# Kernel optimization log

Measured on AMD Instinct MI355X. Metric: run time of the kernel, lower is better.

The kernel has to match this reference:

```python
import jax, jax.numpy as jnp
import numpy as np

B, C, N, H, S = 2048, 64, 64, 8, 4
D = C // H          # head dim 8
CS = C // S         # per-scale channels 16
CP = C // 4         # pattern memory dim 16


def _conv1d(x, w, b):
    # x: [B, Cin, N], w: [Cout, Cin, 3], 'same' padding
    y = jax.lax.conv_general_dilated(x, w, (1,), ((1, 1),),
                                     dimension_numbers=('NCH', 'OIH', 'NCH'))
    return y + b[None, :, None]


def setup_inputs() -> dict:
    key = jax.random.key(0)
    ks = jax.random.split(key, 20)
    s = 0.05
    f32 = jnp.float32
    return {
        'x': jax.random.normal(ks[0], (B, C, N), f32),
        'points': jax.random.normal(ks[1], (N, 3), f32),
        'conv1_w': jax.random.normal(ks[2], (S, CS, C, 3), f32) * s,
        'conv1_b': jnp.zeros((S, CS), f32),
        'conv2_w': jax.random.normal(ks[3], (S, CS, CS, 3), f32) * s,
        'conv2_b': jnp.zeros((S, CS), f32),
        'pattern_memory': jax.random.normal(ks[4], (64, CP), f32),
        'pm1_w': jax.random.normal(ks[5], (C, C + CP), f32) * s,
        'pm1_b': jnp.zeros((C,), f32),
        'pm2_w': jax.random.normal(ks[6], (C, C), f32) * s,
        'pm2_b': jnp.zeros((C,), f32),
        'q_w': jax.random.normal(ks[7], (C, C), f32) * s,
        'q_b': jnp.zeros((C,), f32),
        'k_w': jax.random.normal(ks[8], (C, C), f32) * s,
        'k_b': jnp.zeros((C,), f32),
        'v_w': jax.random.normal(ks[9], (C, C), f32) * s,
        'v_b': jnp.zeros((C,), f32),
        'in_w': jax.random.normal(ks[10], (3 * C, C), f32) * s,
        'in_b': jnp.zeros((3 * C,), f32),
        'mo_w': jax.random.normal(ks[11], (C, C), f32) * s,
        'mo_b': jnp.zeros((C,), f32),
        'out_w': jax.random.normal(ks[12], (C, C), f32) * s,
        'out_b': jnp.zeros((C,), f32),
        'ln_g': jnp.ones((C,), f32),
        'ln_beta': jnp.zeros((C,), f32),
        'adjacency': jax.random.randint(ks[13], (64, 64), 0, 2, jnp.int32),
    }


def _forward(x, points, conv1_w, conv1_b, conv2_w, conv2_b, pattern_memory,
             pm1_w, pm1_b, pm2_w, pm2_b, q_w, q_b, k_w, k_b, v_w, v_b,
             in_w, in_b, mo_w, mo_b, out_w, out_b, ln_g, ln_beta, adjacency):
    b, c, n = x.shape
    # multi-scale conv stacks (fixed small loop over scales)
    feats = []
    for i in range(S):
        y = jax.nn.relu(_conv1d(x, conv1_w[i], conv1_b[i]))
        y = jax.nn.relu(_conv1d(y, conv2_w[i], conv2_b[i]))
        feats.append(jnp.transpose(y, (0, 2, 1)))  # [B, N, CS]
    combined = jnp.concatenate(feats, axis=-1)     # [B, N, C]
    # pattern memory broadcast per point (N == 64)
    pat = jnp.broadcast_to(pattern_memory[None], (b, n, CP))
    pi = jnp.concatenate([combined, pat], axis=-1)  # [B, N, C+CP]
    pf = jax.nn.relu(pi @ pm1_w.T + pm1_b) @ pm2_w.T + pm2_b  # [B, N, C]
    q = pf @ q_w.T + q_b
    k = pf @ k_w.T + k_b
    v = pf @ v_w.T + v_b
    # nn.MultiheadAttention: internal in_proj + out_proj
    wq, wk, wv = in_w[:C], in_w[C:2 * C], in_w[2 * C:]
    bq, bk, bv = in_b[:C], in_b[C:2 * C], in_b[2 * C:]
    q2 = (q @ wq.T + bq).reshape(b, n, H, D)
    k2 = (k @ wk.T + bk).reshape(b, n, H, D)
    v2 = (v @ wv.T + bv).reshape(b, n, H, D)
    scale = 1.0 / np.sqrt(D).astype(np.float32)
    scores = jnp.einsum('bnhd,bmhd->bhnm', q2, k2) * scale
    attn = jax.nn.softmax(scores, axis=-1)
    ctx = jnp.einsum('bhnm,bmhd->bnhd', attn, v2).reshape(b, n, C)
    attended = ctx @ mo_w.T + mo_b
    # vectorized geometric bias (replaces the 64x64 python loop)
    diff = points[:, None, :] - points[None, :, :]
    dist = jnp.sqrt(jnp.sum(diff * diff, axis=-1) + 1e-12)
    geo = jnp.where(adjacency > 0, jnp.float32(0.5), -0.1 / (1.0 + dist))
    attended = attended + geo[None]
    # layer norm over channels, then output projection
    h = attended + pf
    mu = jnp.mean(h, axis=-1, keepdims=True)
    var = jnp.mean((h - mu) ** 2, axis=-1, keepdims=True)
    hn = (h - mu) * jax.lax.rsqrt(var + 1e-5) * ln_g + ln_beta
    out = hn @ out_w.T + out_b
    return jnp.transpose(out, (0, 2, 1))  # [B, C, N]


def reference(x, points, conv1_w, conv1_b, conv2_w, conv2_b, pattern_memory,
              pm1_w, pm1_b, pm2_w, pm2_b, q_w, q_b, k_w, k_b, v_w, v_b,
              in_w, in_b, mo_w, mo_b, out_w, out_b, ln_g, ln_beta, adjacency):
    return _forward(x, points, conv1_w, conv1_b, conv2_w, conv2_b,
                    pattern_memory, pm1_w, pm1_b, pm2_w, pm2_b, q_w, q_b,
                    k_w, k_b, v_w, v_b, in_w, in_b, mo_w, mo_b, out_w, out_b,
                    ln_g, ln_beta, adjacency)
```

## Files before the change

kernel.cpp:

```cpp
#include <hip/hip_runtime.h>
#include <math.h>

using bf16x8 = __attribute__((ext_vector_type(8))) __bf16;
using f32x4  = __attribute__((ext_vector_type(4))) float;

#if __has_builtin(__builtin_amdgcn_exp2f)
#define EXP2F(x) __builtin_amdgcn_exp2f(x)
#else
#define EXP2F(x) exp2f(x)
#endif

__device__ __forceinline__ unsigned short f2bf(float f) {
  unsigned u = __float_as_uint(f);
  unsigned r = u + 0x7fffu + ((u >> 16) & 1u);
  return (unsigned short)(r >> 16);
}

__device__ __forceinline__ unsigned cvt_pk_bf16(float a, float b) {
  unsigned r;
  asm("v_cvt_pk_bf16_f32 %0, %1, %2" : "=v"(r) : "v"(a), "v"(b));
  return r;
}
__device__ __forceinline__ uint2 pk4(float a, float b, float c, float d) {
  uint2 r; r.x = cvt_pk_bf16(a, b); r.y = cvt_pk_bf16(c, d); return r;
}

__device__ __forceinline__ f32x4 mfma16(uint4 a, uint4 b, f32x4 c) {
  return __builtin_amdgcn_mfma_f32_16x16x32_bf16(
      __builtin_bit_cast(bf16x8, a), __builtin_bit_cast(bf16x8, b), c, 0, 0, 0);
}
__device__ __forceinline__ float swz_xor16(float v) {
  return __int_as_float(__builtin_amdgcn_ds_swizzle(__float_as_int(v), 0x401F));
}

#define FRAG_OFF(k, n) (((((n) >> 4) * 2 + ((k) >> 5)) * 64 + (((k) >> 3) & 3) * 16 + ((n) & 15)) * 8 + ((k) & 7))

#define ATT_C 0.51006997f

__global__ void precompute_kernel(
    const float* __restrict__ conv1_w, const float* __restrict__ conv2_w,
    const float* __restrict__ pm1_w, const float* __restrict__ pm1_b,
    const float* __restrict__ pm2_w,
    const float* __restrict__ q_w, const float* __restrict__ q_b,
    const float* __restrict__ k_w, const float* __restrict__ k_b,
    const float* __restrict__ v_w, const float* __restrict__ v_b,
    const float* __restrict__ in_w, const float* __restrict__ in_b,
    const float* __restrict__ mo_w, const float* __restrict__ out_w,
    const float* __restrict__ pattern, const float* __restrict__ points,
    const int* __restrict__ adjacency,
    unsigned short* __restrict__ wsb, float* __restrict__ wsf) {
  int idx = blockIdx.x * 256 + threadIdx.x;
  if (idx < 12288) {
    int t = idx >> 12, rem = idx & 4095;
    int oc = rem >> 6, c = rem & 63;
    wsb[idx] = f2bf(conv1_w[(oc * 64 + c) * 3 + t]);
  } else if (idx < 24576) {
    int i2 = idx - 12288;
    int t = i2 >> 12, rem = i2 & 4095;
    int oc = rem >> 6, ci = rem & 63;
    float v = ((ci >> 4) == (oc >> 4)) ? conv2_w[(oc * 16 + (ci & 15)) * 3 + t] : 0.0f;
    wsb[idx] = f2bf(v);
  } else if (idx < 28672) {
    int rem = idx - 24576;
    wsb[idx] = f2bf(pm1_w[(rem >> 6) * 80 + (rem & 63)]);
  } else if (idx < 32768) {
    wsb[idx] = f2bf(pm2_w[idx - 28672]);
  } else if (idx < 36864) {
    int rem = idx - 32768; int c = rem >> 6, k = rem & 63;
    float s = 0.f;
    #pragma unroll 8
    for (int j = 0; j < 64; ++j) s += in_w[c * 64 + j] * q_w[j * 64 + k];
    wsb[idx] = f2bf(s * ATT_C);
  } else if (idx < 40960) {
    int rem = idx - 36864; int c = rem >> 6, k = rem & 63;
    float s = 0.f;
    #pragma unroll 8
    for (int j = 0; j < 64; ++j) s += in_w[(64 + c) * 64 + j] * k_w[j * 64 + k];
    wsb[idx] = f2bf(s);
  } else if (idx < 45056) {
    int rem = idx - 40960; int c = rem >> 6, k = rem & 63;
    float s = 0.f;
    #pragma unroll 8
    for (int j = 0; j < 64; ++j) s += in_w[(128 + c) * 64 + j] * v_w[j * 64 + k];
    wsb[idx] = f2bf(s);
  } else if (idx < 49152) {
    wsb[idx] = f2bf(mo_w[idx - 45056]);
  } else if (idx < 53248) {
    wsb[idx] = f2bf(out_w[idx - 49152]);
  } else if (idx < 57344) {
    int rem = idx - 53248; int t = rem >> 4, j = rem & 15;
    int wq = t >> 6, lq = (t >> 4) & 3, l15 = t & 15;
    int c = wq * 16 + lq * 4 + (j & 3);
    int n = (j >> 2) * 16 + l15;
    float s = pm1_b[c];
    #pragma unroll
    for (int cp = 0; cp < 16; ++cp) s += pm1_w[c * 80 + 64 + cp] * pattern[n * 16 + cp];
    wsf[rem] = s;
  } else if (idx < 61440) {
    int rem = idx - 57344; int t = rem >> 4, j = rem & 15;
    int wq = t >> 6, lq = (t >> 4) & 3, l15 = t & 15;
    int c = wq * 16 + lq * 4 + (j & 3);
    int n = (j >> 2) * 16 + l15;
    float dd = 1e-12f;
    #pragma unroll
    for (int i = 0; i < 3; ++i) { float d = points[n * 3 + i] - points[c * 3 + i]; dd += d * d; }
    float dist = sqrtf(dd);
    wsf[4096 + rem] = (adjacency[n * 64 + c] > 0) ? 0.5f : (-0.1f / (1.0f + dist));
  } else if (idx < 61632) {
    int rem = idx - 61440; int which = rem >> 6, c = rem & 63;
    if (which == 0) {
      float s = in_b[c];
      for (int j = 0; j < 64; ++j) s += in_w[c * 64 + j] * q_b[j];
      wsf[8192 + c] = s * ATT_C;
    } else if (which == 1) {
      float s = in_b[64 + c];
      for (int j = 0; j < 64; ++j) s += in_w[(64 + c) * 64 + j] * k_b[j];
      wsf[8256 + c] = s;
    } else {
      float s = in_b[128 + c];
      for (int j = 0; j < 64; ++j) s += in_w[(128 + c) * 64 + j] * v_b[j];
      wsf[8320 + c] = s;
    }
  }
}

__device__ __forceinline__ void gemm64r(const bf16x8 a[2], const unsigned short* Bf,
                                        int lane, f32x4 acc[4]) {
  #pragma unroll
  for (int s = 0; s < 2; ++s) {
    #pragma unroll
    for (int nt = 0; nt < 4; ++nt) {
      bf16x8 bb = *reinterpret_cast<const bf16x8*>(Bf + ((nt * 2 + s) * 64 + lane) * 8);
      acc[nt] = __builtin_amdgcn_mfma_f32_16x16x32_bf16(a[s], bb, acc[nt], 0, 0, 0);
    }
  }
}

#define SLOT_B 4096
#define KBASE  8704
#define VBASE  13312
#define H32F   2048

__global__ __launch_bounds__(256, 4) void fused_kernel(
    const float* __restrict__ x,
    const unsigned short* __restrict__ wsb, const float* __restrict__ wsf,
    const float* __restrict__ conv1_b, const float* __restrict__ conv2_b,
    const float* __restrict__ pm2_b, const float* __restrict__ mo_b,
    const float* __restrict__ out_b, const float* __restrict__ ln_g,
    const float* __restrict__ ln_beta, float* __restrict__ out) {
  __shared__ __align__(16) unsigned char smem_raw[35840];
  unsigned short* S16 = reinterpret_cast<unsigned short*>(smem_raw);
  float* S32 = reinterpret_cast<float*>(smem_raw);

  const int tid = threadIdx.x;
  const int b = blockIdx.x;
  const int lane = tid & 63;
  const int w = tid >> 6;
  const int l15 = lane & 15;
  const int lq = lane >> 4;
  const int c0 = 16 * w + lq * 4;
  f32x4 pfs[4];

  auto ldw = [&](int off) -> bf16x8 {
    return *reinterpret_cast<const bf16x8*>(wsb + off + (16 * w + l15) * 64 + lq * 8);
  };

  bf16x8 a6[3][2];
  bf16x8 pA[2], pB[2];
  f32x4 cp4[4], gd4[4];
  f32x4 bq4, bk4, mo_b4, ob4;
  float bvv[4];

  if (tid < 8) S16[VBASE + tid] = 0;
  {
    const float* xb = x + b * 4096 + w * 16 * 64 + lane;
    float v[16];
    #pragma unroll
    for (int j = 0; j < 16; ++j) v[j] = xb[j * 64];
    #pragma unroll
    for (int g = 0; g < 2; ++g) {
      uint4 u;
      u.x = cvt_pk_bf16(v[g * 8 + 0], v[g * 8 + 1]);
      u.y = cvt_pk_bf16(v[g * 8 + 2], v[g * 8 + 3]);
      u.z = cvt_pk_bf16(v[g * 8 + 4], v[g * 8 + 5]);
      u.w = cvt_pk_bf16(v[g * 8 + 6], v[g * 8 + 7]);
      *reinterpret_cast<uint4*>(S16 + FRAG_OFF(w * 16 + g * 8, lane)) = u;
    }
  }
  #pragma unroll
  for (int t = 0; t < 3; ++t) { a6[t][0] = ldw(t * 4096); a6[t][1] = ldw(t * 4096 + 32); }
  f32x4 c1b = *reinterpret_cast<const f32x4*>(conv1_b + c0);
  __syncthreads();

  auto conv_pass = [&](int srcBase, f32x4 acc[4]) {
    #pragma unroll
    for (int nt = 0; nt < 4; ++nt) {
      #pragma unroll
      for (int t = 0; t < 3; ++t) {
        int np = nt * 16 + l15 + (t - 1);
        bool ok = (unsigned)np < 64u;
        int a = srcBase + (((np >> 4) * 2) * 64 + lq * 16 + (np & 15)) * 8;
        int A0 = ok ? a : VBASE;
        int A1 = ok ? (a + 512) : VBASE;
        bf16x8 b0 = *reinterpret_cast<const bf16x8*>(S16 + A0);
        bf16x8 b1 = *reinterpret_cast<const bf16x8*>(S16 + A1);
        acc[nt] = __builtin_amdgcn_mfma_f32_16x16x32_bf16(a6[t][0], b0, acc[nt], 0, 0, 0);
        acc[nt] = __builtin_amdgcn_mfma_f32_16x16x32_bf16(a6[t][1], b1, acc[nt], 0, 0, 0);
      }
    }
  };

  {
    f32x4 acc[4] = {};
    conv_pass(0, acc);
    #pragma unroll
    for (int nt = 0; nt < 4; ++nt) {
      int n = nt * 16 + l15;
      uint2 u = pk4(fmaxf(acc[nt][0] + c1b[0], 0.f), fmaxf(acc[nt][1] + c1b[1], 0.f),
                    fmaxf(acc[nt][2] + c1b[2], 0.f), fmaxf(acc[nt][3] + c1b[3], 0.f));
      *reinterpret_cast<uint2*>(S16 + SLOT_B + FRAG_OFF(c0, n)) = u;
    }
  }
  #pragma unroll
  for (int t = 0; t < 3; ++t) { a6[t][0] = ldw(12288 + t * 4096); a6[t][1] = ldw(12288 + t * 4096 + 32); }
  f32x4 c2b = *reinterpret_cast<const f32x4*>(conv2_b + c0);
  __syncthreads();

  {
    f32x4 acc[4] = {};
    conv_pass(SLOT_B, acc);
    #pragma unroll
    for (int nt = 0; nt < 4; ++nt) {
      int n = nt * 16 + l15;
      uint2 u = pk4(fmaxf(acc[nt][0] + c2b[0], 0.f), fmaxf(acc[nt][1] + c2b[1], 0.f),
                    fmaxf(acc[nt][2] + c2b[2], 0.f), fmaxf(acc[nt][3] + c2b[3], 0.f));
      *reinterpret_cast<uint2*>(S16 + FRAG_OFF(c0, n)) = u;
    }
  }
  pA[0] = ldw(24576); pA[1] = ldw(24576 + 32);
  #pragma unroll
  for (int k2 = 0; k2 < 4; ++k2)
    cp4[k2] = *reinterpret_cast<const f32x4*>(wsf + tid * 16 + k2 * 4);
  __syncthreads();

  {
    f32x4 acc[4] = {};
    gemm64r(pA, S16, lane, acc);
    #pragma unroll
    for (int nt = 0; nt < 4; ++nt) {
      int n = nt * 16 + l15;
      uint2 u = pk4(fmaxf(acc[nt][0] + cp4[nt][0], 0.f),
                    fmaxf(acc[nt][1] + cp4[nt][1], 0.f),
                    fmaxf(acc[nt][2] + cp4[nt][2], 0.f),
                    fmaxf(acc[nt][3] + cp4[nt][3], 0.f));
      *reinterpret_cast<uint2*>(S16 + SLOT_B + FRAG_OFF(c0, n)) = u;
    }
  }
  pA[0] = ldw(28672); pA[1] = ldw(28672 + 32);
  f32x4 p2b = *reinterpret_cast<const f32x4*>(pm2_b + c0);
  __syncthreads();

  {
    f32x4 acc[4] = {};
    gemm64r(pA, S16 + SLOT_B, lane, acc);
    #pragma unroll
    for (int nt = 0; nt < 4; ++nt) {
      int n = nt * 16 + l15;
      f32x4 v;
      #pragma unroll
      for (int r = 0; r < 4; ++r) v[r] = acc[nt][r] + p2b[r];
      pfs[nt] = v;
      *reinterpret_cast<uint2*>(S16 + FRAG_OFF(c0, n)) = pk4(v[0], v[1], v[2], v[3]);
    }
  }
  pA[0] = ldw(32768); pA[1] = ldw(32768 + 32);
  pB[0] = ldw(36864); pB[1] = ldw(36864 + 32);
  bq4 = *reinterpret_cast<const f32x4*>(wsf + 8192 + c0);
  bk4 = *reinterpret_cast<const f32x4*>(wsf + 8256 + c0);
  #pragma unroll
  for (int ct = 0; ct < 4; ++ct) bvv[ct] = wsf[8320 + ct * 16 + l15];
  __syncthreads();

  {
    f32x4 acc[4] = {};
    gemm64r(pA, S16, lane, acc);
    #pragma unroll
    for (int nt = 0; nt < 4; ++nt) {
      int n = nt * 16 + l15;
      *reinterpret_cast<uint2*>(S16 + SLOT_B + n * 72 + c0) =
          pk4(acc[nt][0] + bq4[0], acc[nt][1] + bq4[1],
              acc[nt][2] + bq4[2], acc[nt][3] + bq4[3]);
    }
  }
  {
    f32x4 acc[4] = {};
    gemm64r(pB, S16, lane, acc);
    #pragma unroll
    for (int nt = 0; nt < 4; ++nt) {
      int n = nt * 16 + l15;
      *reinterpret_cast<uint2*>(S16 + KBASE + n * 72 + c0) =
          pk4(acc[nt][0] + bk4[0], acc[nt][1] + bk4[1],
              acc[nt][2] + bk4[2], acc[nt][3] + bk4[3]);
    }
  }
  {
    f32x4 acc[4] = {};
    const unsigned short* AV = wsb + 40960;
    #pragma unroll
    for (int s = 0; s < 2; ++s) {
      bf16x8 a = *reinterpret_cast<const bf16x8*>(S16 + ((w * 2 + s) * 64 + lane) * 8);
      #pragma unroll
      for (int ct = 0; ct < 4; ++ct) {
        bf16x8 bb = *reinterpret_cast<const bf16x8*>(
            AV + (ct * 16 + l15) * 64 + s * 32 + lq * 8);
        acc[ct] = __builtin_amdgcn_mfma_f32_16x16x32_bf16(a, bb, acc[ct], 0, 0, 0);
      }
    }
    const int m0 = 16 * w + lq * 4;
    #pragma unroll
    for (int ct = 0; ct < 4; ++ct) {
      int c = ct * 16 + l15;
      float bia = bvv[ct];
      *reinterpret_cast<uint2*>(S16 + VBASE + c * 72 + m0) =
          pk4(acc[ct][0] + bia, acc[ct][1] + bia, acc[ct][2] + bia, acc[ct][3] + bia);
    }
  }
  __syncthreads();

  {
    const bool lq0 = (lq == 0);
    uint4 vb[2][2], ka[2][4];
    #pragma unroll
    for (int rr = 0; rr < 2; ++rr) {
      const int h = w + rr * 4;
      #pragma unroll
      for (int ks = 0; ks < 2; ++ks)
        vb[rr][ks] = *reinterpret_cast<const uint4*>(
            S16 + VBASE + (h * 8 + (l15 & 7)) * 72 + ks * 32 + lq * 8);
      #pragma unroll
      for (int mt = 0; mt < 4; ++mt) {
        uint4 t = *reinterpret_cast<const uint4*>(
            S16 + KBASE + (mt * 16 + l15) * 72 + h * 8);
        ka[rr][mt].x = lq0 ? t.x : 0u; ka[rr][mt].y = lq0 ? t.y : 0u;
        ka[rr][mt].z = lq0 ? t.z : 0u; ka[rr][mt].w = lq0 ? t.w : 0u;
      }
    }
    __syncthreads();

    float invb[2];
    auto stageA = [&](int i) {
      const int rr = i >> 2, q = i & 3;
      const int h = w + rr * 4;
      uint4 qb = *reinterpret_cast<const uint4*>(
          S16 + SLOT_B + (q * 16 + l15) * 72 + h * 8);
      f32x4 sc[4];
      #pragma unroll
      for (int mt = 0; mt < 4; ++mt) {
        f32x4 z = {0.f, 0.f, 0.f, 0.f};
        sc[mt] = mfma16(ka[rr][mt], qb, z);
      }
      float sum = 0.f;
      #pragma unroll
      for (int mt = 0; mt < 4; ++mt)
        #pragma unroll
        for (int r = 0; r < 4; ++r) {
          float e = EXP2F(sc[mt][r]);
          sc[mt][r] = e; sum += e;
        }
      const int Pb = KBASE + (w * 2 + (i & 1)) * 1152;
      #pragma unroll
      for (int mt = 0; mt < 4; ++mt) {
        unsigned d0 = __builtin_amdgcn_perm(__float_as_uint(sc[mt][1]),
                                            __float_as_uint(sc[mt][0]), 0x07060302u);
        unsigned d1 = __builtin_amdgcn_perm(__float_as_uint(sc[mt][3]),
                                            __float_as_uint(sc[mt][2]), 0x07060302u);
        *reinterpret_cast<uint2*>(S16 + Pb + l15 * 72 + mt * 16 + lq * 4) =
            make_uint2(d0, d1);
      }
      sum += swz_xor16(sum);
      sum += __shfl_xor(sum, 32);
      invb[i & 1] = __builtin_amdgcn_rcpf(sum);
    };
    auto stageB = [&](int i) {
      const int rr = i >> 2, q = i & 3;
      const int Pb = KBASE + (w * 2 + (i & 1)) * 1152;
      const float inv = invb[i & 1];
      f32x4 ctx = {0.f, 0.f, 0.f, 0.f};
      #pragma unroll
      for (int ks = 0; ks < 2; ++ks) {
        uint4 pa = *reinterpret_cast<const uint4*>(
            S16 + Pb + l15 * 72 + ks * 32 + lq * 8);
        ctx = mfma16(pa, vb[rr][ks], ctx);
      }
      if (l15 < 8) {
        const int kk = (w + rr * 4) * 8 + l15;
        #pragma unroll
        for (int r = 0; r < 4; ++r)
          S16[FRAG_OFF(kk, q * 16 + lq * 4 + r)] = f2bf(ctx[r] * inv);
      }
    };
    stageA(0);
    #pragma unroll
    for (int i = 0; i < 8; ++i) {
      if (i < 7) stageA(i + 1);
      stageB(i);
    }
  }
  pA[0] = ldw(45056); pA[1] = ldw(45056 + 32);
  mo_b4 = *reinterpret_cast<const f32x4*>(mo_b + c0);
  #pragma unroll
  for (int k2 = 0; k2 < 4; ++k2)
    gd4[k2] = *reinterpret_cast<const f32x4*>(wsf + 4096 + tid * 16 + k2 * 4);
  __syncthreads();

  {
    f32x4 acc[4] = {};
    gemm64r(pA, S16, lane, acc);
    #pragma unroll
    for (int nt = 0; nt < 4; ++nt) {
      int n = nt * 16 + l15;
      #pragma unroll
      for (int r = 0; r < 4; ++r) {
        int c = c0 + r;
        S32[H32F + c * 65 + n] = acc[nt][r] + mo_b4[r] + gd4[nt][r] + pfs[nt][r];
      }
    }
  }
  __syncthreads();

  {
    const int n = 16 * w + l15;
    const int ch0 = lq * 16;
    f32x4 g0 = *reinterpret_cast<const f32x4*>(ln_g + ch0);
    f32x4 g1 = *reinterpret_cast<const f32x4*>(ln_g + ch0 + 4);
    f32x4 g2 = *reinterpret_cast<const f32x4*>(ln_g + ch0 + 8);
    f32x4 g3 = *reinterpret_cast<const f32x4*>(ln_g + ch0 + 12);
    f32x4 e0 = *reinterpret_cast<const f32x4*>(ln_beta + ch0);
    f32x4 e1 = *reinterpret_cast<const f32x4*>(ln_beta + ch0 + 4);
    f32x4 e2 = *reinterpret_cast<const f32x4*>(ln_beta + ch0 + 8);
    f32x4 e3 = *reinterpret_cast<const f32x4*>(ln_beta + ch0 + 12);
    float sum = 0.f, ssq = 0.f;
    float hv[16];
    #pragma unroll
    for (int j = 0; j < 16; ++j) {
      float v = S32[H32F + (ch0 + j) * 65 + n];
      hv[j] = v; sum += v; ssq += v * v;
    }
    sum += swz_xor16(sum);  sum += __shfl_xor(sum, 32);
    ssq += swz_xor16(ssq);  ssq += __shfl_xor(ssq, 32);
    float mu = sum * (1.0f / 64.0f);
    float rs = rsqrtf(ssq * (1.0f / 64.0f) - mu * mu + 1e-5f);
    float gg[16] = {g0[0],g0[1],g0[2],g0[3], g1[0],g1[1],g1[2],g1[3],
                    g2[0],g2[1],g2[2],g2[3], g3[0],g3[1],g3[2],g3[3]};
    float ee[16] = {e0[0],e0[1],e0[2],e0[3], e1[0],e1[1],e1[2],e1[3],
                    e2[0],e2[1],e2[2],e2[3], e3[0],e3[1],e3[2],e3[3]};
    #pragma unroll
    for (int half = 0; half < 2; ++half) {
      float vv[8];
      #pragma unroll
      for (int jj = 0; jj < 8; ++jj) {
        int j = half * 8 + jj;
        vv[jj] = (hv[j] - mu) * rs * gg[j] + ee[j];
      }
      uint4 u;
      u.x = cvt_pk_bf16(vv[0], vv[1]);
      u.y = cvt_pk_bf16(vv[2], vv[3]);
      u.z = cvt_pk_bf16(vv[4], vv[5]);
      u.w = cvt_pk_bf16(vv[6], vv[7]);
      *reinterpret_cast<uint4*>(S16 + FRAG_OFF(ch0 + half * 8, n)) = u;
    }
  }
  pA[0] = ldw(49152); pA[1] = ldw(49152 + 32);
  ob4 = *reinterpret_cast<const f32x4*>(out_b + c0);
  __syncthreads();

  {
    f32x4 acc[4] = {};
    gemm64r(pA, S16, lane, acc);
    float* ob = out + b * 4096;
    #pragma unroll
    for (int nt = 0; nt < 4; ++nt) {
      int n = nt * 16 + l15;
      #pragma unroll
      for (int r = 0; r < 4; ++r)
        ob[(c0 + r) * 64 + n] = acc[nt][r] + ob4[r];
    }
  }
}

extern "C" void kernel_launch(void* const* d_in, const int* in_sizes, int n_in,
                              void* d_out, int out_size, void* d_ws, size_t ws_size,
                              hipStream_t stream) {
  const float* x        = (const float*)d_in[0];
  const float* points   = (const float*)d_in[1];
  const float* conv1_w  = (const float*)d_in[2];
  const float* conv1_b  = (const float*)d_in[3];
  const float* conv2_w  = (const float*)d_in[4];
  const float* conv2_b  = (const float*)d_in[5];
  const float* pattern  = (const float*)d_in[6];
  const float* pm1_w    = (const float*)d_in[7];
  const float* pm1_b    = (const float*)d_in[8];
  const float* pm2_w    = (const float*)d_in[9];
  const float* pm2_b    = (const float*)d_in[10];
  const float* q_w      = (const float*)d_in[11];
  const float* q_b      = (const float*)d_in[12];
  const float* k_w      = (const float*)d_in[13];
  const float* k_b      = (const float*)d_in[14];
  const float* v_w      = (const float*)d_in[15];
  const float* v_b      = (const float*)d_in[16];
  const float* in_w     = (const float*)d_in[17];
  const float* in_b     = (const float*)d_in[18];
  const float* mo_w     = (const float*)d_in[19];
  const float* mo_b     = (const float*)d_in[20];
  const float* out_w    = (const float*)d_in[21];
  const float* out_b    = (const float*)d_in[22];
  const float* ln_g     = (const float*)d_in[23];
  const float* ln_beta  = (const float*)d_in[24];
  const int*   adjacency= (const int*)d_in[25];

  unsigned short* wsb = (unsigned short*)d_ws;
  float* wsf = (float*)((char*)d_ws + 106496);

  precompute_kernel<<<241, 256, 0, stream>>>(
      conv1_w, conv2_w, pm1_w, pm1_b, pm2_w, q_w, q_b, k_w, k_b, v_w, v_b,
      in_w, in_b, mo_w, out_w, pattern, points, adjacency, wsb, wsf);

  fused_kernel<<<2048, 256, 0, stream>>>(
      x, wsb, wsf, conv1_b, conv2_b, pm2_b, mo_b, out_b, ln_g, ln_beta,
      (float*)d_out);
}
```

Baseline: 167.2 us.

## Process two batch items per workgroup to amortize weight loads and syncs

Each workgroup now handles two batch samples, keeping two copies of every shared-memory buffer. Weight fragments loaded into registers and the barriers are shared across both samples, and the attention loop interleaves them for more independent MFMA work. The grid is halved and LDS per block doubles to 70KB, while launch bounds drop to 2 blocks per CU. This risks lower occupancy and higher register pressure.

```diff
diff --git a/kernel.cpp b/kernel.cpp
--- a/kernel.cpp
+++ b/kernel.cpp
@@ -136,19 +136,21 @@
   }
 }
 
+#define POOL   17920
+#define POOLF  8960
 #define SLOT_B 4096
 #define KBASE  8704
 #define VBASE  13312
 #define H32F   2048
 
-__global__ __launch_bounds__(256, 4) void fused_kernel(
+__global__ __launch_bounds__(256, 2) void fused_kernel(
     const float* __restrict__ x,
     const unsigned short* __restrict__ wsb, const float* __restrict__ wsf,
     const float* __restrict__ conv1_b, const float* __restrict__ conv2_b,
     const float* __restrict__ pm2_b, const float* __restrict__ mo_b,
     const float* __restrict__ out_b, const float* __restrict__ ln_g,
     const float* __restrict__ ln_beta, float* __restrict__ out) {
-  __shared__ __align__(16) unsigned char smem_raw[35840];
+  __shared__ __align__(16) unsigned char smem_raw[71680];
   unsigned short* S16 = reinterpret_cast<unsigned short*>(smem_raw);
   float* S32 = reinterpret_cast<float*>(smem_raw);
 
@@ -159,7 +161,7 @@
   const int l15 = lane & 15;
   const int lq = lane >> 4;
   const int c0 = 16 * w + lq * 4;
-  f32x4 pfs[4];
+  f32x4 pfs[2][4];
 
   auto ldw = [&](int off) -> bf16x8 {
     return *reinterpret_cast<const bf16x8*>(wsb + off + (16 * w + l15) * 64 + lq * 8);
@@ -171,9 +173,10 @@
   f32x4 bq4, bk4, mo_b4, ob4;
   float bvv[4];
 
-  if (tid < 8) S16[VBASE + tid] = 0;
-  {
-    const float* xb = x + b * 4096 + w * 16 * 64 + lane;
+  if (tid < 8) { S16[VBASE + tid] = 0; S16[POOL + VBASE + tid] = 0; }
+  #pragma unroll
+  for (int bb = 0; bb < 2; ++bb) {
+    const float* xb = x + (2 * b + bb) * 4096 + w * 16 * 64 + lane;
     float v[16];
     #pragma unroll
     for (int j = 0; j < 16; ++j) v[j] = xb[j * 64];
@@ -184,7 +187,7 @@
       u.y = cvt_pk_bf16(v[g * 8 + 2], v[g * 8 + 3]);
       u.z = cvt_pk_bf16(v[g * 8 + 4], v[g * 8 + 5]);
       u.w = cvt_pk_bf16(v[g * 8 + 6], v[g * 8 + 7]);
-      *reinterpret_cast<uint4*>(S16 + FRAG_OFF(w * 16 + g * 8, lane)) = u;
+      *reinterpret_cast<uint4*>(S16 + bb * POOL + FRAG_OFF(w * 16 + g * 8, lane)) = u;
     }
   }
   #pragma unroll
@@ -192,7 +195,7 @@
   f32x4 c1b = *reinterpret_cast<const f32x4*>(conv1_b + c0);
   __syncthreads();
 
-  auto conv_pass = [&](int srcBase, f32x4 acc[4]) {
+  auto conv_pass = [&](const unsigned short* Sb, int srcBase, f32x4 acc[4]) {
     #pragma unroll
     for (int nt = 0; nt < 4; ++nt) {
       #pragma unroll
@@ -202,8 +205,8 @@
         int a = srcBase + (((np >> 4) * 2) * 64 + lq * 16 + (np & 15)) * 8;
         int A0 = ok ? a : VBASE;
         int A1 = ok ? (a + 512) : VBASE;
-        bf16x8 b0 = *reinterpret_cast<const bf16x8*>(S16 + A0);
-        bf16x8 b1 = *reinterpret_cast<const bf16x8*>(S16 + A1);
+        bf16x8 b0 = *reinterpret_cast<const bf16x8*>(Sb + A0);
+        bf16x8 b1 = *reinterpret_cast<const bf16x8*>(Sb + A1);
         acc[nt] = __builtin_amdgcn_mfma_f32_16x16x32_bf16(a6[t][0], b0, acc[nt], 0, 0, 0);
         acc[nt] = __builtin_amdgcn_mfma_f32_16x16x32_bf16(a6[t][1], b1, acc[nt], 0, 0, 0);
       }
@@ -211,14 +214,18 @@
   };
 
   {
-    f32x4 acc[4] = {};
-    conv_pass(0, acc);
-    #pragma unroll
-    for (int nt = 0; nt < 4; ++nt) {
-      int n = nt * 16 + l15;
-      uint2 u = pk4(fmaxf(acc[nt][0] + c1b[0], 0.f), fmaxf(acc[nt][1] + c1b[1], 0.f),
-                    fmaxf(acc[nt][2] + c1b[2], 0.f), fmaxf(acc[nt][3] + c1b[3], 0.f));
-      *reinterpret_cast<uint2*>(S16 + SLOT_B + FRAG_OFF(c0, n)) = u;
+    f32x4 a0[4] = {}, a1[4] = {};
+    conv_pass(S16, 0, a0);
+    conv_pass(S16 + POOL, 0, a1);
+    #pragma unroll
+    for (int nt = 0; nt < 4; ++nt) {
+      int n = nt * 16 + l15;
+      *reinterpret_cast<uint2*>(S16 + SLOT_B + FRAG_OFF(c0, n)) =
+          pk4(fmaxf(a0[nt][0] + c1b[0], 0.f), fmaxf(a0[nt][1] + c1b[1], 0.f),
+              fmaxf(a0[nt][2] + c1b[2], 0.f), fmaxf(a0[nt][3] + c1b[3], 0.f));
+      *reinterpret_cast<uint2*>(S16 + POOL + SLOT_B + FRAG_OFF(c0, n)) =
+          pk4(fmaxf(a1[nt][0] + c1b[0], 0.f), fmaxf(a1[nt][1] + c1b[1], 0.f),
+              fmaxf(a1[nt][2] + c1b[2], 0.f), fmaxf(a1[nt][3] + c1b[3], 0.f));
     }
   }
   #pragma unroll
@@ -227,14 +234,18 @@
   __syncthreads();
 
   {
-    f32x4 acc[4] = {};
-    conv_pass(SLOT_B, acc);
-    #pragma unroll
-    for (int nt = 0; nt < 4; ++nt) {
-      int n = nt * 16 + l15;
-      uint2 u = pk4(fmaxf(acc[nt][0] + c2b[0], 0.f), fmaxf(acc[nt][1] + c2b[1], 0.f),
-                    fmaxf(acc[nt][2] + c2b[2], 0.f), fmaxf(acc[nt][3] + c2b[3], 0.f));
-      *reinterpret_cast<uint2*>(S16 + FRAG_OFF(c0, n)) = u;
+    f32x4 a0[4] = {}, a1[4] = {};
+    conv_pass(S16, SLOT_B, a0);
+    conv_pass(S16 + POOL, SLOT_B, a1);
+    #pragma unroll
+    for (int nt = 0; nt < 4; ++nt) {
+      int n = nt * 16 + l15;
+      *reinterpret_cast<uint2*>(S16 + FRAG_OFF(c0, n)) =
+          pk4(fmaxf(a0[nt][0] + c2b[0], 0.f), fmaxf(a0[nt][1] + c2b[1], 0.f),
+              fmaxf(a0[nt][2] + c2b[2], 0.f), fmaxf(a0[nt][3] + c2b[3], 0.f));
+      *reinterpret_cast<uint2*>(S16 + POOL + FRAG_OFF(c0, n)) =
+          pk4(fmaxf(a1[nt][0] + c2b[0], 0.f), fmaxf(a1[nt][1] + c2b[1], 0.f),
+              fmaxf(a1[nt][2] + c2b[2], 0.f), fmaxf(a1[nt][3] + c2b[3], 0.f));
     }
   }
   pA[0] = ldw(24576); pA[1] = ldw(24576 + 32);
@@ -244,16 +255,18 @@
   __syncthreads();
 
   {
-    f32x4 acc[4] = {};
-    gemm64r(pA, S16, lane, acc);
-    #pragma unroll
-    for (int nt = 0; nt < 4; ++nt) {
-      int n = nt * 16 + l15;
-      uint2 u = pk4(fmaxf(acc[nt][0] + cp4[nt][0], 0.f),
-                    fmaxf(acc[nt][1] + cp4[nt][1], 0.f),
-                    fmaxf(acc[nt][2] + cp4[nt][2], 0.f),
-                    fmaxf(acc[nt][3] + cp4[nt][3], 0.f));
-      *reinterpret_cast<uint2*>(S16 + SLOT_B + FRAG_OFF(c0, n)) = u;
+    f32x4 a0[4] = {}, a1[4] = {};
+    gemm64r(pA, S16, lane, a0);
+    gemm64r(pA, S16 + POOL, lane, a1);
+    #pragma unroll
+    for (int nt = 0; nt < 4; ++nt) {
+      int n = nt * 16 + l15;
+      *reinterpret_cast<uint2*>(S16 + SLOT_B + FRAG_OFF(c0, n)) =
+          pk4(fmaxf(a0[nt][0] + cp4[nt][0], 0.f), fmaxf(a0[nt][1] + cp4[nt][1], 0.f),
+              fmaxf(a0[nt][2] + cp4[nt][2], 0.f), fmaxf(a0[nt][3] + cp4[nt][3], 0.f));
+      *reinterpret_cast<uint2*>(S16 + POOL + SLOT_B + FRAG_OFF(c0, n)) =
+          pk4(fmaxf(a1[nt][0] + cp4[nt][0], 0.f), fmaxf(a1[nt][1] + cp4[nt][1], 0.f),
+              fmaxf(a1[nt][2] + cp4[nt][2], 0.f), fmaxf(a1[nt][3] + cp4[nt][3], 0.f));
     }
   }
   pA[0] = ldw(28672); pA[1] = ldw(28672 + 32);
@@ -261,16 +274,18 @@
   __syncthreads();
 
   {
-    f32x4 acc[4] = {};
-    gemm64r(pA, S16 + SLOT_B, lane, acc);
-    #pragma unroll
-    for (int nt = 0; nt < 4; ++nt) {
-      int n = nt * 16 + l15;
-      f32x4 v;
-      #pragma unroll
-      for (int r = 0; r < 4; ++r) v[r] = acc[nt][r] + p2b[r];
-      pfs[nt] = v;
-      *reinterpret_cast<uint2*>(S16 + FRAG_OFF(c0, n)) = pk4(v[0], v[1], v[2], v[3]);
+    f32x4 a0[4] = {}, a1[4] = {};
+    gemm64r(pA, S16 + SLOT_B, lane, a0);
+    gemm64r(pA, S16 + POOL + SLOT_B, lane, a1);
+    #pragma unroll
+    for (int nt = 0; nt < 4; ++nt) {
+      int n = nt * 16 + l15;
+      f32x4 v0, v1;
+      #pragma unroll
+      for (int r = 0; r < 4; ++r) { v0[r] = a0[nt][r] + p2b[r]; v1[r] = a1[nt][r] + p2b[r]; }
+      pfs[0][nt] = v0; pfs[1][nt] = v1;
+      *reinterpret_cast<uint2*>(S16 + FRAG_OFF(c0, n)) = pk4(v0[0], v0[1], v0[2], v0[3]);
+      *reinterpret_cast<uint2*>(S16 + POOL + FRAG_OFF(c0, n)) = pk4(v1[0], v1[1], v1[2], v1[3]);
     }
   }
   pA[0] = ldw(32768); pA[1] = ldw(32768 + 32);
@@ -282,82 +297,94 @@
   __syncthreads();
 
   {
-    f32x4 acc[4] = {};
-    gemm64r(pA, S16, lane, acc);
+    f32x4 a0[4] = {}, a1[4] = {};
+    gemm64r(pA, S16, lane, a0);
+    gemm64r(pA, S16 + POOL, lane, a1);
     #pragma unroll
     for (int nt = 0; nt < 4; ++nt) {
       int n = nt * 16 + l15;
       *reinterpret_cast<uint2*>(S16 + SLOT_B + n * 72 + c0) =
-          pk4(acc[nt][0] + bq4[0], acc[nt][1] + bq4[1],
-              acc[nt][2] + bq4[2], acc[nt][3] + bq4[3]);
-    }
-  }
-  {
-    f32x4 acc[4] = {};
-    gemm64r(pB, S16, lane, acc);
+          pk4(a0[nt][0] + bq4[0], a0[nt][1] + bq4[1], a0[nt][2] + bq4[2], a0[nt][3] + bq4[3]);
+      *reinterpret_cast<uint2*>(S16 + POOL + SLOT_B + n * 72 + c0) =
+          pk4(a1[nt][0] + bq4[0], a1[nt][1] + bq4[1], a1[nt][2] + bq4[2], a1[nt][3] + bq4[3]);
+    }
+  }
+  {
+    f32x4 a0[4] = {}, a1[4] = {};
+    gemm64r(pB, S16, lane, a0);
+    gemm64r(pB, S16 + POOL, lane, a1);
     #pragma unroll
     for (int nt = 0; nt < 4; ++nt) {
       int n = nt * 16 + l15;
       *reinterpret_cast<uint2*>(S16 + KBASE + n * 72 + c0) =
-          pk4(acc[nt][0] + bk4[0], acc[nt][1] + bk4[1],
-              acc[nt][2] + bk4[2], acc[nt][3] + bk4[3]);
-    }
-  }
-  {
-    f32x4 acc[4] = {};
+          pk4(a0[nt][0] + bk4[0], a0[nt][1] + bk4[1], a0[nt][2] + bk4[2], a0[nt][3] + bk4[3]);
+      *reinterpret_cast<uint2*>(S16 + POOL + KBASE + n * 72 + c0) =
+          pk4(a1[nt][0] + bk4[0], a1[nt][1] + bk4[1], a1[nt][2] + bk4[2], a1[nt][3] + bk4[3]);
+    }
+  }
+  {
+    bf16x8 av[2][4];
     const unsigned short* AV = wsb + 40960;
     #pragma unroll
-    for (int s = 0; s < 2; ++s) {
-      bf16x8 a = *reinterpret_cast<const bf16x8*>(S16 + ((w * 2 + s) * 64 + lane) * 8);
+    for (int s = 0; s < 2; ++s)
+      #pragma unroll
+      for (int ct = 0; ct < 4; ++ct)
+        av[s][ct] = *reinterpret_cast<const bf16x8*>(AV + (ct * 16 + l15) * 64 + s * 32 + lq * 8);
+    const int m0 = 16 * w + lq * 4;
+    #pragma unroll
+    for (int bb = 0; bb < 2; ++bb) {
+      f32x4 acc[4] = {};
+      #pragma unroll
+      for (int s = 0; s < 2; ++s) {
+        bf16x8 a = *reinterpret_cast<const bf16x8*>(S16 + bb * POOL + ((w * 2 + s) * 64 + lane) * 8);
+        #pragma unroll
+        for (int ct = 0; ct < 4; ++ct)
+          acc[ct] = __builtin_amdgcn_mfma_f32_16x16x32_bf16(a, av[s][ct], acc[ct], 0, 0, 0);
+      }
       #pragma unroll
       for (int ct = 0; ct < 4; ++ct) {
-        bf16x8 bb = *reinterpret_cast<const bf16x8*>(
-            AV + (ct * 16 + l15) * 64 + s * 32 + lq * 8);
-        acc[ct] = __builtin_amdgcn_mfma_f32_16x16x32_bf16(a, bb, acc[ct], 0, 0, 0);
-      }
-    }
-    const int m0 = 16 * w + lq * 4;
-    #pragma unroll
-    for (int ct = 0; ct < 4; ++ct) {
-      int c = ct * 16 + l15;
-      float bia = bvv[ct];
-      *reinterpret_cast<uint2*>(S16 + VBASE + c * 72 + m0) =
-          pk4(acc[ct][0] + bia, acc[ct][1] + bia, acc[ct][2] + bia, acc[ct][3] + bia);
+        int c = ct * 16 + l15;
+        float bia = bvv[ct];
+        *reinterpret_cast<uint2*>(S16 + bb * POOL + VBASE + c * 72 + m0) =
+            pk4(acc[ct][0] + bia, acc[ct][1] + bia, acc[ct][2] + bia, acc[ct][3] + bia);
+      }
     }
   }
   __syncthreads();
 
   {
     const bool lq0 = (lq == 0);
-    uint4 vb[2][2], ka[2][4];
-    #pragma unroll
-    for (int rr = 0; rr < 2; ++rr) {
-      const int h = w + rr * 4;
-      #pragma unroll
-      for (int ks = 0; ks < 2; ++ks)
-        vb[rr][ks] = *reinterpret_cast<const uint4*>(
-            S16 + VBASE + (h * 8 + (l15 & 7)) * 72 + ks * 32 + lq * 8);
-      #pragma unroll
-      for (int mt = 0; mt < 4; ++mt) {
-        uint4 t = *reinterpret_cast<const uint4*>(
-            S16 + KBASE + (mt * 16 + l15) * 72 + h * 8);
-        ka[rr][mt].x = lq0 ? t.x : 0u; ka[rr][mt].y = lq0 ? t.y : 0u;
-        ka[rr][mt].z = lq0 ? t.z : 0u; ka[rr][mt].w = lq0 ? t.w : 0u;
-      }
-    }
+    uint4 vb[2][2][2], ka[2][2][4];
+    #pragma unroll
+    for (int bb = 0; bb < 2; ++bb)
+      #pragma unroll
+      for (int rr = 0; rr < 2; ++rr) {
+        const int h = w + rr * 4;
+        #pragma unroll
+        for (int ks = 0; ks < 2; ++ks)
+          vb[bb][rr][ks] = *reinterpret_cast<const uint4*>(
+              S16 + bb * POOL + VBASE + (h * 8 + (l15 & 7)) * 72 + ks * 32 + lq * 8);
+        #pragma unroll
+        for (int mt = 0; mt < 4; ++mt) {
+          uint4 t = *reinterpret_cast<const uint4*>(
+              S16 + bb * POOL + KBASE + (mt * 16 + l15) * 72 + h * 8);
+          ka[bb][rr][mt].x = lq0 ? t.x : 0u; ka[bb][rr][mt].y = lq0 ? t.y : 0u;
+          ka[bb][rr][mt].z = lq0 ? t.z : 0u; ka[bb][rr][mt].w = lq0 ? t.w : 0u;
+        }
+      }
     __syncthreads();
 
     float invb[2];
     auto stageA = [&](int i) {
-      const int rr = i >> 2, q = i & 3;
+      const int bb = i & 1, j = i >> 1, rr = j >> 2, q = j & 3;
       const int h = w + rr * 4;
       uint4 qb = *reinterpret_cast<const uint4*>(
-          S16 + SLOT_B + (q * 16 + l15) * 72 + h * 8);
+          S16 + bb * POOL + SLOT_B + (q * 16 + l15) * 72 + h * 8);
       f32x4 sc[4];
       #pragma unroll
       for (int mt = 0; mt < 4; ++mt) {
         f32x4 z = {0.f, 0.f, 0.f, 0.f};
-        sc[mt] = mfma16(ka[rr][mt], qb, z);
+        sc[mt] = mfma16(ka[bb][rr][mt], qb, z);
       }
       float sum = 0.f;
       #pragma unroll
@@ -367,7 +394,7 @@
           float e = EXP2F(sc[mt][r]);
           sc[mt][r] = e; sum += e;
         }
-      const int Pb = KBASE + (w * 2 + (i & 1)) * 1152;
+      const int Pb = bb * POOL + KBASE + (w * 2 + ((i >> 1) & 1)) * 1152;
       #pragma unroll
       for (int mt = 0; mt < 4; ++mt) {
         unsigned d0 = __builtin_amdgcn_perm(__float_as_uint(sc[mt][1]),
@@ -382,27 +409,27 @@
       invb[i & 1] = __builtin_amdgcn_rcpf(sum);
     };
     auto stageB = [&](int i) {
-      const int rr = i >> 2, q = i & 3;
-      const int Pb = KBASE + (w * 2 + (i & 1)) * 1152;
+      const int bb = i & 1, j = i >> 1, rr = j >> 2, q = j & 3;
+      const int Pb = bb * POOL + KBASE + (w * 2 + ((i >> 1) & 1)) * 1152;
       const float inv = invb[i & 1];
       f32x4 ctx = {0.f, 0.f, 0.f, 0.f};
       #pragma unroll
       for (int ks = 0; ks < 2; ++ks) {
         uint4 pa = *reinterpret_cast<const uint4*>(
             S16 + Pb + l15 * 72 + ks * 32 + lq * 8);
-        ctx = mfma16(pa, vb[rr][ks], ctx);
+        ctx = mfma16(pa, vb[bb][rr][ks], ctx);
       }
       if (l15 < 8) {
         const int kk = (w + rr * 4) * 8 + l15;
         #pragma unroll
         for (int r = 0; r < 4; ++r)
-          S16[FRAG_OFF(kk, q * 16 + lq * 4 + r)] = f2bf(ctx[r] * inv);
+          S16[bb * POOL + FRAG_OFF(kk, q * 16 + lq * 4 + r)] = f2bf(ctx[r] * inv);
       }
     };
     stageA(0);
     #pragma unroll
-    for (int i = 0; i < 8; ++i) {
-      if (i < 7) stageA(i + 1);
+    for (int i = 0; i < 16; ++i) {
+      if (i < 15) stageA(i + 1);
       stageB(i);
     }
   }
@@ -414,15 +441,17 @@
   __syncthreads();
 
   {
-    f32x4 acc[4] = {};
-    gemm64r(pA, S16, lane, acc);
+    f32x4 a0[4] = {}, a1[4] = {};
+    gemm64r(pA, S16, lane, a0);
+    gemm64r(pA, S16 + POOL, lane, a1);
     #pragma unroll
     for (int nt = 0; nt < 4; ++nt) {
       int n = nt * 16 + l15;
       #pragma unroll
       for (int r = 0; r < 4; ++r) {
         int c = c0 + r;
-        S32[H32F + c * 65 + n] = acc[nt][r] + mo_b4[r] + gd4[nt][r] + pfs[nt][r];
+        S32[H32F + c * 65 + n] = a0[nt][r] + mo_b4[r] + gd4[nt][r] + pfs[0][nt][r];
+        S32[POOLF + H32F + c * 65 + n] = a1[nt][r] + mo_b4[r] + gd4[nt][r] + pfs[1][nt][r];
       }
     }
   }
@@ -439,35 +468,38 @@
     f32x4 e1 = *reinterpret_cast<const f32x4*>(ln_beta + ch0 + 4);
     f32x4 e2 = *reinterpret_cast<const f32x4*>(ln_beta + ch0 + 8);
     f32x4 e3 = *reinterpret_cast<const f32x4*>(ln_beta + ch0 + 12);
-    float sum = 0.f, ssq = 0.f;
-    float hv[16];
-    #pragma unroll
-    for (int j = 0; j < 16; ++j) {
-      float v = S32[H32F + (ch0 + j) * 65 + n];
-      hv[j] = v; sum += v; ssq += v * v;
-    }
-    sum += swz_xor16(sum);  sum += __shfl_xor(sum, 32);
-    ssq += swz_xor16(ssq);  ssq += __shfl_xor(ssq, 32);
-    float mu = sum * (1.0f / 64.0f);
-    float rs = rsqrtf(ssq * (1.0f / 64.0f) - mu * mu + 1e-5f);
     float gg[16] = {g0[0],g0[1],g0[2],g0[3], g1[0],g1[1],g1[2],g1[3],
                     g2[0],g2[1],g2[2],g2[3], g3[0],g3[1],g3[2],g3[3]};
     float ee[16] = {e0[0],e0[1],e0[2],e0[3], e1[0],e1[1],e1[2],e1[3],
                     e2[0],e2[1],e2[2],e2[3], e3[0],e3[1],e3[2],e3[3]};
     #pragma unroll
-    for (int half = 0; half < 2; ++half) {
-      float vv[8];
-      #pragma unroll
-      for (int jj = 0; jj < 8; ++jj) {
-        int j = half * 8 + jj;
-        vv[jj] = (hv[j] - mu) * rs * gg[j] + ee[j];
-      }
-      uint4 u;
-      u.x = cvt_pk_bf16(vv[0], vv[1]);
-      u.y = cvt_pk_bf16(vv[2], vv[3]);
-      u.z = cvt_pk_bf16(vv[4], vv[5]);
-      u.w = cvt_pk_bf16(vv[6], vv[7]);
-      *reinterpret_cast<uint4*>(S16 + FRAG_OFF(ch0 + half * 8, n)) = u;
+    for (int bb = 0; bb < 2; ++bb) {
+      float sum = 0.f, ssq = 0.f;
+      float hv[16];
+      #pragma unroll
+      for (int j = 0; j < 16; ++j) {
+        float v = S32[bb * POOLF + H32F + (ch0 + j) * 65 + n];
+        hv[j] = v; sum += v; ssq += v * v;
+      }
+      sum += swz_xor16(sum);  sum += __shfl_xor(sum, 32);
+      ssq += swz_xor16(ssq);  ssq += __shfl_xor(ssq, 32);
+      float mu = sum * (1.0f / 64.0f);
+      float rs = rsqrtf(ssq * (1.0f / 64.0f) - mu * mu + 1e-5f);
+      #pragma unroll
+      for (int half = 0; half < 2; ++half) {
+        float vv[8];
+        #pragma unroll
+        for (int jj = 0; jj < 8; ++jj) {
+          int j = half * 8 + jj;
+          vv[jj] = (hv[j] - mu) * rs * gg[j] + ee[j];
+        }
+        uint4 u;
+        u.x = cvt_pk_bf16(vv[0], vv[1]);
+        u.y = cvt_pk_bf16(vv[2], vv[3]);
+        u.z = cvt_pk_bf16(vv[4], vv[5]);
+        u.w = cvt_pk_bf16(vv[6], vv[7]);
+        *reinterpret_cast<uint4*>(S16 + bb * POOL + FRAG_OFF(ch0 + half * 8, n)) = u;
+      }
     }
   }
   pA[0] = ldw(49152); pA[1] = ldw(49152 + 32);
@@ -475,15 +507,19 @@
   __syncthreads();
 
   {
-    f32x4 acc[4] = {};
-    gemm64r(pA, S16, lane, acc);
-    float* ob = out + b * 4096;
-    #pragma unroll
-    for (int nt = 0; nt < 4; ++nt) {
-      int n = nt * 16 + l15;
-      #pragma unroll
-      for (int r = 0; r < 4; ++r)
-        ob[(c0 + r) * 64 + n] = acc[nt][r] + ob4[r];
+    f32x4 a0[4] = {}, a1[4] = {};
+    gemm64r(pA, S16, lane, a0);
+    gemm64r(pA, S16 + POOL, lane, a1);
+    float* ob0 = out + (2 * b) * 4096;
+    float* ob1 = out + (2 * b + 1) * 4096;
+    #pragma unroll
+    for (int nt = 0; nt < 4; ++nt) {
+      int n = nt * 16 + l15;
+      #pragma unroll
+      for (int r = 0; r < 4; ++r) {
+        ob0[(c0 + r) * 64 + n] = a0[nt][r] + ob4[r];
+        ob1[(c0 + r) * 64 + n] = a1[nt][r] + ob4[r];
+      }
     }
   }
 }
@@ -525,7 +561,7 @@
       conv1_w, conv2_w, pm1_w, pm1_b, pm2_w, q_w, q_b, k_w, k_b, v_w, v_b,
       in_w, in_b, mo_w, out_w, pattern, points, adjacency, wsb, wsf);
 
-  fused_kernel<<<2048, 256, 0, stream>>>(
+  fused_kernel<<<1024, 256, 0, stream>>>(
       x, wsb, wsf, conv1_b, conv2_b, pm2_b, mo_b, out_b, ln_g, ln_beta,
       (float*)d_out);
 }
```

Result: no change. 165.6 us (-0.9%).
